# Kernel tuning notes

Hardware: AMD Instinct MI355X
Metric: run time of the kernel (lower is better)

Reference implementation:

```python
import jax, jax.numpy as jnp
import numpy as np

N_NODES = 50000
N_EDGES = 800000
D = 128


def _gcn_conv(x, edge_index, W, b):
    """PyG GCNConv: out = D^{-1/2} (A + I) D^{-1/2} (x W) + b.

    edge_index[0] = source nodes, edge_index[1] = target nodes.
    Self-loops handled analytically instead of materializing them.
    """
    n = x.shape[0]
    src, dst = edge_index[0], edge_index[1]
    h = x @ W  # [N, out]
    # degree with self-loop: in-degree of target + 1
    deg = jax.ops.segment_sum(jnp.ones_like(dst, dtype=h.dtype), dst, num_segments=n) + 1.0
    dinv = jax.lax.rsqrt(deg)  # deg >= 1, safe
    norm = dinv[src] * dinv[dst]  # [E]
    msgs = norm[:, None] * h[src]  # [E, out]  (the big irregular-gather intermediate)
    agg = jax.ops.segment_sum(msgs, dst, num_segments=n)
    # self-loop contribution: norm = dinv[i]*dinv[i] = 1/deg
    agg = agg + h * (1.0 / deg)[:, None]
    return agg + b


def setup_inputs() -> dict:
    key = jax.random.key(0)
    k1, k2, k3, k4 = jax.random.split(key, 4)
    x = jax.random.normal(k1, (N_NODES, D), dtype=jnp.float32)
    edge_index = jax.random.randint(k2, (2, N_EDGES), 0, N_NODES, dtype=jnp.int64)
    scale = 1.0 / np.sqrt(D)
    W1 = jax.random.normal(k3, (D, D), dtype=jnp.float32) * scale
    W2 = jax.random.normal(k4, (D, D), dtype=jnp.float32) * scale
    b1 = jnp.zeros((D,), dtype=jnp.float32)
    b2 = jnp.zeros((D,), dtype=jnp.float32)
    return {"x": x, "edge_index": edge_index, "W1": W1, "b1": b1, "W2": W2, "b2": b2}


def reference(x, edge_index, W1, b1, W2, b2):
    h = _gcn_conv(x, edge_index, W1, b1)
    h = jax.nn.relu(h)  # dropout p=0.0 -> identity
    out = _gcn_conv(h, edge_index, W2, b2)
    return out
```

## Files before the change

### kernel.cpp

```cpp
#include <hip/hip_runtime.h>

#define DF 128
#define NBKT_MAX 256
#define CAP 8192
#define SCHUNK 2048

typedef unsigned int uint;
typedef unsigned short ushort;
typedef __attribute__((ext_vector_type(8))) short short8;
typedef __attribute__((ext_vector_type(4))) float f32x4;

union frag_u { uint4 u4; short8 s8; };

__device__ __forceinline__ uint f2u(float f) { return __float_as_uint(f); }
__device__ __forceinline__ ushort rne_bf16(float v) {
    uint u = __float_as_uint(v);
    u = u + 0x7FFFu + ((u >> 16) & 1u);
    return (ushort)(u >> 16);
}
__device__ __forceinline__ float bflo(uint u) { return __uint_as_float(u << 16); }
__device__ __forceinline__ float bfhi(uint u) { return __uint_as_float(u & 0xFFFF0000u); }

__global__ __launch_bounds__(256) void scatter_wprep(const int* __restrict__ src,
                                                     const int* __restrict__ dst,
                                                     int* __restrict__ ccur,
                                                     uint* __restrict__ ebuf,
                                                     int E, int NB, int SB,
                                                     const float* __restrict__ W1,
                                                     const float* __restrict__ W2,
                                                     uint4* __restrict__ Whi,
                                                     uint4* __restrict__ Wlo) {
    __shared__ int cnt[NBKT_MAX];
    __shared__ int base[NBKT_MAX];
    int t = threadIdx.x;
    if ((int)blockIdx.x < SB) {
        int e0 = blockIdx.x * SCHUNK;
        int eb0 = e0 + t * 8;
        int lim = min(E - eb0, 8);
        int d[8], s[8];
        if (lim == 8) {
            int4 d0 = *(const int4*)(dst + eb0), d1 = *(const int4*)(dst + eb0 + 4);
            int4 s0 = *(const int4*)(src + eb0), s1 = *(const int4*)(src + eb0 + 4);
            d[0] = d0.x; d[1] = d0.y; d[2] = d0.z; d[3] = d0.w;
            d[4] = d1.x; d[5] = d1.y; d[6] = d1.z; d[7] = d1.w;
            s[0] = s0.x; s[1] = s0.y; s[2] = s0.z; s[3] = s0.w;
            s[4] = s1.x; s[5] = s1.y; s[6] = s1.z; s[7] = s1.w;
        } else {
            for (int i = 0; i < 8; ++i) { d[i] = 0; s[i] = 0; }
            for (int i = 0; i < lim; ++i) { d[i] = dst[eb0 + i]; s[i] = src[eb0 + i]; }
        }
        for (int i = t; i < NB; i += 256) cnt[i] = 0;
        __syncthreads();
        for (int i = 0; i < 8; ++i)
            if (i < lim) atomicAdd(&cnt[d[i] >> 8], 1);
        __syncthreads();
        for (int i = t; i < NB; i += 256) base[i] = cnt[i] ? atomicAdd(&ccur[i], cnt[i]) : 0;
        __syncthreads();
        for (int i = 0; i < 8; ++i)
            if (i < lim) {
                int b = d[i] >> 8;
                int pos = atomicAdd(&base[b], 1);
                if (pos < CAP) ebuf[(size_t)b * CAP + pos] = ((uint)(d[i] & 255) << 24) | (uint)s[i];
            }
    } else {
        int tt4 = ((int)blockIdx.x - SB) * 256 + t;
        int wsel = tt4 >> 11;
        int tt = tt4 & 2047;
        const float* W = wsel ? W2 : W1;
        int lane = tt & 63;
        int n  = ((tt >> 6) & 7) * 16 + (lane & 15);
        int k0 = (tt >> 9) * 32 + (lane >> 4) * 8;
        uint hi[4], lo[4];
#pragma unroll
        for (int p = 0; p < 4; ++p) {
            float f0 = W[(size_t)(k0 + 2 * p) * DF + n];
            float f1 = W[(size_t)(k0 + 2 * p + 1) * DF + n];
            uint u0 = f2u(f0), u1 = f2u(f1);
            hi[p] = (u1 & 0xFFFF0000u) | (u0 >> 16);
            float l0 = f0 - __uint_as_float(u0 & 0xFFFF0000u);
            float l1 = f1 - __uint_as_float(u1 & 0xFFFF0000u);
            lo[p] = (f2u(l1) & 0xFFFF0000u) | (f2u(l0) >> 16);
        }
        Whi[wsel * 2048 + tt] = make_uint4(hi[0], hi[1], hi[2], hi[3]);
        Wlo[wsel * 2048 + tt] = make_uint4(lo[0], lo[1], lo[2], lo[3]);
    }
}

__global__ __launch_bounds__(256) void sort_gemm1(const uint* __restrict__ ebuf,
                                                  const int* __restrict__ ccur,
                                                  int* __restrict__ rstart,
                                                  int* __restrict__ rend,
                                                  float* __restrict__ dinv,
                                                  ushort* __restrict__ srcs,
                                                  const float* __restrict__ A,
                                                  const uint4* __restrict__ Bhi,
                                                  const uint4* __restrict__ Blo,
                                                  ushort* __restrict__ Hq,
                                                  int NB, int N) {
    __shared__ int cnt[256];
    __shared__ int sp[256];
    int t = threadIdx.x;
    if ((int)blockIdx.x < NB) {
        int b = blockIdx.x;
        int count = min(ccur[b], CAP);
        const uint* eb = ebuf + (size_t)b * CAP;
        cnt[t] = 0;
        __syncthreads();
        for (int j = t; j < count; j += 256) atomicAdd(&cnt[eb[j] >> 24], 1);
        __syncthreads();
        int v = cnt[t];
        int pv = (v + 7) & ~7;
        sp[t] = pv;
        __syncthreads();
        for (int off = 1; off < 256; off <<= 1) {
            int x = (t >= off) ? sp[t - off] : 0;
            __syncthreads();
            sp[t] += x;
            __syncthreads();
        }
        int ex = sp[t] - pv;
        int node = b * 256 + t;
        if (node < N) {
            rstart[node] = b * CAP + ex;
            rend[node]   = b * CAP + ex + v;
            dinv[node] = rsqrtf((float)v + 1.0f);
        }
        sp[t] = ex;
        __syncthreads();
        for (int j = t; j < count; j += 256) {
            uint e = eb[j];
            int pos = atomicAdd(&sp[e >> 24], 1);
            if (pos < CAP) srcs[(size_t)b * CAP + pos] = (ushort)(e & 0xFFFFFFu);
        }
    } else {
        const int lane = t & 63;
        const int w = t >> 6;
        const int l15 = lane & 15, quad = lane >> 4;
        const int rowbase = ((int)blockIdx.x - NB) * 128 + w * 32;
        const int M = N;

        f32x4 acc[2][8];
#pragma unroll
        for (int rt = 0; rt < 2; ++rt)
#pragma unroll
            for (int ct = 0; ct < 8; ++ct) acc[rt][ct] = (f32x4){0.f, 0.f, 0.f, 0.f};

        for (int q = 0; q < 4; ++q) {
            frag_u ah[2], al[2];
#pragma unroll
            for (int rt = 0; rt < 2; ++rt) {
                int m = rowbase + rt * 16 + l15;
                if (m >= M) m = M - 1;
                const float* ap = A + (size_t)m * DF + q * 32 + quad * 8;
                float4 v0 = *(const float4*)ap;
                float4 v1 = *(const float4*)(ap + 4);
                float f[8] = {v0.x, v0.y, v0.z, v0.w, v1.x, v1.y, v1.z, v1.w};
                uint hi[4], lo[4];
#pragma unroll
                for (int p = 0; p < 4; ++p) {
                    uint u0 = f2u(f[2 * p]), u1 = f2u(f[2 * p + 1]);
                    hi[p] = (u1 & 0xFFFF0000u) | (u0 >> 16);
                    float l0 = f[2 * p]     - __uint_as_float(u0 & 0xFFFF0000u);
                    float l1 = f[2 * p + 1] - __uint_as_float(u1 & 0xFFFF0000u);
                    lo[p] = (f2u(l1) & 0xFFFF0000u) | (f2u(l0) >> 16);
                }
                ah[rt].u4 = make_uint4(hi[0], hi[1], hi[2], hi[3]);
                al[rt].u4 = make_uint4(lo[0], lo[1], lo[2], lo[3]);
            }
#pragma unroll
            for (int ct = 0; ct < 8; ++ct) {
                frag_u bh, bl;
                bh.u4 = Bhi[(q * 8 + ct) * 64 + lane];
                bl.u4 = Blo[(q * 8 + ct) * 64 + lane];
#pragma unroll
                for (int rt = 0; rt < 2; ++rt) {
                    acc[rt][ct] = __builtin_amdgcn_mfma_f32_16x16x32_bf16(al[rt].s8, bh.s8, acc[rt][ct], 0, 0, 0);
                    acc[rt][ct] = __builtin_amdgcn_mfma_f32_16x16x32_bf16(ah[rt].s8, bl.s8, acc[rt][ct], 0, 0, 0);
                    acc[rt][ct] = __builtin_amdgcn_mfma_f32_16x16x32_bf16(ah[rt].s8, bh.s8, acc[rt][ct], 0, 0, 0);
                }
            }
        }
#pragma unroll
        for (int rt = 0; rt < 2; ++rt)
#pragma unroll
            for (int reg = 0; reg < 4; ++reg) {
                int row = rowbase + rt * 16 + quad * 4 + reg;
                if (row < M) {
#pragma unroll
                    for (int ct = 0; ct < 8; ++ct)
                        Hq[((size_t)(ct >> 1) * M + row) * 32 + (ct & 1) * 16 + l15] =
                            rne_bf16(acc[rt][ct][reg]);
                }
            }
    }
}

__global__ __launch_bounds__(256) void gemm_bf16A(const ushort* __restrict__ A,
                                                  const uint4* __restrict__ Bhi,
                                                  const uint4* __restrict__ Blo,
                                                  const float* __restrict__ dinv,
                                                  ushort* __restrict__ Hq, int M) {
    const int lane = threadIdx.x & 63;
    const int w = threadIdx.x >> 6;
    const int l15 = lane & 15, quad = lane >> 4;
    const int rowbase = blockIdx.x * 128 + w * 32;

    f32x4 acc[2][8];
#pragma unroll
    for (int rt = 0; rt < 2; ++rt)
#pragma unroll
        for (int ct = 0; ct < 8; ++ct) acc[rt][ct] = (f32x4){0.f, 0.f, 0.f, 0.f};

    for (int q = 0; q < 4; ++q) {
        frag_u a[2];
#pragma unroll
        for (int rt = 0; rt < 2; ++rt) {
            int m = rowbase + rt * 16 + l15;
            if (m >= M) m = M - 1;
            const ushort* ap = A + ((size_t)q * M + m) * 32 + quad * 8;
            a[rt].u4 = *(const uint4*)ap;
        }
#pragma unroll
        for (int ct = 0; ct < 8; ++ct) {
            frag_u bh, bl;
            bh.u4 = Bhi[(q * 8 + ct) * 64 + lane];
            bl.u4 = Blo[(q * 8 + ct) * 64 + lane];
#pragma unroll
            for (int rt = 0; rt < 2; ++rt) {
                acc[rt][ct] = __builtin_amdgcn_mfma_f32_16x16x32_bf16(a[rt].s8, bl.s8, acc[rt][ct], 0, 0, 0);
                acc[rt][ct] = __builtin_amdgcn_mfma_f32_16x16x32_bf16(a[rt].s8, bh.s8, acc[rt][ct], 0, 0, 0);
            }
        }
    }
#pragma unroll
    for (int rt = 0; rt < 2; ++rt)
#pragma unroll
        for (int reg = 0; reg < 4; ++reg) {
            int row = rowbase + rt * 16 + quad * 4 + reg;
            if (row < M) {
                float di = dinv[row];
#pragma unroll
                for (int ct = 0; ct < 8; ++ct)
                    Hq[((size_t)(ct >> 1) * M + row) * 32 + (ct & 1) * 16 + l15] =
                        rne_bf16(acc[rt][ct][reg] * di);
            }
        }
}

template<bool L1>
__global__ __launch_bounds__(256) void quarter_gather(const uint4* __restrict__ H4,
                                                      const float* __restrict__ dinv,
                                                      const int* __restrict__ rstart,
                                                      const int* __restrict__ rend,
                                                      const ushort* __restrict__ srcs,
                                                      const float* __restrict__ bias,
                                                      void* __restrict__ outv, int N) {
    int t = threadIdx.x;
    int bid = blockIdx.x;
    int sub = bid & 7;
    int q = sub >> 1;
    int n = (bid >> 3) * 128 + (sub & 1) * 64 + (t >> 2);
    if (n >= N) return;
    int l = t & 3;
    const uint4* Hq4 = H4 + (size_t)q * N * 4;

    float4 bb0 = ((const float4*)bias)[q * 8 + l * 2];
    float4 bb1 = ((const float4*)bias)[q * 8 + l * 2 + 1];

    float di = dinv[n];
    uint4 self = Hq4[(size_t)n * 4 + l];
    float sc = L1 ? di : 1.0f;
    float a0 = bflo(self.x) * sc, a1 = bfhi(self.x) * sc, a2 = bflo(self.y) * sc, a3 = bfhi(self.y) * sc;
    float a4 = bflo(self.z) * sc, a5 = bfhi(self.z) * sc, a6 = bflo(self.w) * sc, a7 = bfhi(self.w) * sc;

    int j = rstart[n], end = rend[n];
    for (; j + 8 <= end; j += 8) {
        uint4 sv = *(const uint4*)(srcs + j);
        int si[8];
        si[0] = sv.x & 0xFFFF; si[1] = sv.x >> 16;
        si[2] = sv.y & 0xFFFF; si[3] = sv.y >> 16;
        si[4] = sv.z & 0xFFFF; si[5] = sv.z >> 16;
        si[6] = sv.w & 0xFFFF; si[7] = sv.w >> 16;
        uint4 v[8];
#pragma unroll
        for (int i = 0; i < 8; ++i) v[i] = Hq4[(size_t)si[i] * 4 + l];
        if constexpr (L1) {
            float dd[8];
#pragma unroll
            for (int i = 0; i < 8; ++i) dd[i] = dinv[si[i]];
#pragma unroll
            for (int i = 0; i < 8; ++i) {
                a0 = fmaf(bflo(v[i].x), dd[i], a0); a1 = fmaf(bfhi(v[i].x), dd[i], a1);
                a2 = fmaf(bflo(v[i].y), dd[i], a2); a3 = fmaf(bfhi(v[i].y), dd[i], a3);
                a4 = fmaf(bflo(v[i].z), dd[i], a4); a5 = fmaf(bfhi(v[i].z), dd[i], a5);
                a6 = fmaf(bflo(v[i].w), dd[i], a6); a7 = fmaf(bfhi(v[i].w), dd[i], a7);
            }
        } else {
#pragma unroll
            for (int i = 0; i < 8; ++i) {
                a0 += bflo(v[i].x); a1 += bfhi(v[i].x);
                a2 += bflo(v[i].y); a3 += bfhi(v[i].y);
                a4 += bflo(v[i].z); a5 += bfhi(v[i].z);
                a6 += bflo(v[i].w); a7 += bfhi(v[i].w);
            }
        }
    }
    for (; j < end; ++j) {
        int s = srcs[j];
        uint4 v = Hq4[(size_t)s * 4 + l];
        if constexpr (L1) {
            float d = dinv[s];
            a0 = fmaf(bflo(v.x), d, a0); a1 = fmaf(bfhi(v.x), d, a1);
            a2 = fmaf(bflo(v.y), d, a2); a3 = fmaf(bfhi(v.y), d, a3);
            a4 = fmaf(bflo(v.z), d, a4); a5 = fmaf(bfhi(v.z), d, a5);
            a6 = fmaf(bflo(v.w), d, a6); a7 = fmaf(bfhi(v.w), d, a7);
        } else {
            a0 += bflo(v.x); a1 += bfhi(v.x); a2 += bflo(v.y); a3 += bfhi(v.y);
            a4 += bflo(v.z); a5 += bfhi(v.z); a6 += bflo(v.w); a7 += bfhi(v.w);
        }
    }
    float o0 = fmaf(a0, di, bb0.x), o1 = fmaf(a1, di, bb0.y);
    float o2 = fmaf(a2, di, bb0.z), o3 = fmaf(a3, di, bb0.w);
    float o4 = fmaf(a4, di, bb1.x), o5 = fmaf(a5, di, bb1.y);
    float o6 = fmaf(a6, di, bb1.z), o7 = fmaf(a7, di, bb1.w);
    if (L1) {
        o0 = fmaxf(o0, 0.f); o1 = fmaxf(o1, 0.f); o2 = fmaxf(o2, 0.f); o3 = fmaxf(o3, 0.f);
        o4 = fmaxf(o4, 0.f); o5 = fmaxf(o5, 0.f); o6 = fmaxf(o6, 0.f); o7 = fmaxf(o7, 0.f);
        uint4 pk;
        pk.x = (uint)rne_bf16(o0) | ((uint)rne_bf16(o1) << 16);
        pk.y = (uint)rne_bf16(o2) | ((uint)rne_bf16(o3) << 16);
        pk.z = (uint)rne_bf16(o4) | ((uint)rne_bf16(o5) << 16);
        pk.w = (uint)rne_bf16(o6) | ((uint)rne_bf16(o7) << 16);
        ((uint4*)outv)[((size_t)q * N + n) * 4 + l] = pk;
    } else {
        float4* op = (float4*)((float*)outv + (size_t)n * DF + q * 32 + l * 8);
        op[0] = make_float4(o0, o1, o2, o3);
        op[1] = make_float4(o4, o5, o6, o7);
    }
}

extern "C" void kernel_launch(void* const* d_in, const int* in_sizes, int n_in,
                              void* d_out, int out_size, void* d_ws, size_t ws_size,
                              hipStream_t stream) {
    const float* x  = (const float*)d_in[0];
    const int*   ei = (const int*)d_in[1];
    const float* W1 = (const float*)d_in[2];
    const float* b1 = (const float*)d_in[3];
    const float* W2 = (const float*)d_in[4];
    const float* b2 = (const float*)d_in[5];

    const int N = in_sizes[0] / DF;
    const int E = in_sizes[1] / 2;
    const int* src = ei;
    const int* dstp = ei + E;
    const int NB = (N + 255) >> 8;
    const int SB = (E + SCHUNK - 1) / SCHUNK;

    float* out = (float*)d_out;
    char* ws = (char*)d_ws;
    size_t off = 0;
    auto carve = [&](size_t bytes) { void* p = ws + off; off += (bytes + 255) & ~(size_t)255; return p; };
    ushort* Hq     = (ushort*)carve((size_t)N * DF * sizeof(ushort));
    ushort* Z1     = (ushort*)carve((size_t)N * DF * sizeof(ushort));
    float*  dinv   = (float*)carve((size_t)N * sizeof(float));
    int*    rstart = (int*)carve((size_t)N * sizeof(int));
    int*    rend   = (int*)carve((size_t)N * sizeof(int));
    uint*   ebuf   = (uint*)carve((size_t)NB * CAP * sizeof(uint));
    ushort* srcs   = (ushort*)carve((size_t)NB * CAP * sizeof(ushort));
    int*    ccur   = (int*)carve(NBKT_MAX * sizeof(int));
    uint4*  Whi    = (uint4*)carve(2 * 2048 * sizeof(uint4));
    uint4*  Wlo    = (uint4*)carve(2 * 2048 * sizeof(uint4));

    const int gemm_b = (N + 127) / 128;
    const int gath_b = ((N + 127) / 128) * 8;

    hipMemsetAsync(ccur, 0, NBKT_MAX * sizeof(int), stream);
    scatter_wprep<<<SB + 16, 256, 0, stream>>>(src, dstp, ccur, ebuf, E, NB, SB, W1, W2, Whi, Wlo);

    sort_gemm1<<<NB + gemm_b, 256, 0, stream>>>(ebuf, ccur, rstart, rend, dinv, srcs,
                                                x, Whi, Wlo, Hq, NB, N);

    quarter_gather<true><<<gath_b, 256, 0, stream>>>((const uint4*)Hq, dinv, rstart, rend,
                                                     srcs, b1, Z1, N);

    gemm_bf16A<<<gemm_b, 256, 0, stream>>>(Z1, Whi + 2048, Wlo + 2048, dinv, Hq, N);
    quarter_gather<false><<<gath_b, 256, 0, stream>>>((const uint4*)Hq, dinv, rstart, rend,
                                                      srcs, b2, out, N);
}
```

Baseline: 201.3 us.

## Precompute per-edge source dinv in CSR order and split sort into two passes

The bucket sort is split into two kernels, each co-scheduled with half of the first GEMM's blocks. The second pass also writes a per-edge array holding dinv of each source node alongside srcs. The layer-1 gather then reads these contiguous normalisation factors as float4 vectors instead of doing a random dinv lookup per edge, and it prefetches the next group of source indices. This removes irregular dinv gathers at the cost of an extra kernel launch, an extra per-edge float array to write and read, and a re-read of ebuf.

```diff
diff --git a/kernel.cpp b/kernel.cpp
--- a/kernel.cpp
+++ b/kernel.cpp
@@ -86,17 +86,81 @@
     }
 }
 
-__global__ __launch_bounds__(256) void sort_gemm1(const uint* __restrict__ ebuf,
-                                                  const int* __restrict__ ccur,
-                                                  int* __restrict__ rstart,
-                                                  int* __restrict__ rend,
-                                                  float* __restrict__ dinv,
-                                                  ushort* __restrict__ srcs,
-                                                  const float* __restrict__ A,
-                                                  const uint4* __restrict__ Bhi,
-                                                  const uint4* __restrict__ Blo,
-                                                  ushort* __restrict__ Hq,
-                                                  int NB, int N) {
+__device__ __forceinline__ void gemm1_body(int gb, int t,
+                                           const float* __restrict__ A,
+                                           const uint4* __restrict__ Bhi,
+                                           const uint4* __restrict__ Blo,
+                                           ushort* __restrict__ Hq, int M) {
+    const int lane = t & 63;
+    const int w = t >> 6;
+    const int l15 = lane & 15, quad = lane >> 4;
+    const int rowbase = gb * 128 + w * 32;
+
+    f32x4 acc[2][8];
+#pragma unroll
+    for (int rt = 0; rt < 2; ++rt)
+#pragma unroll
+        for (int ct = 0; ct < 8; ++ct) acc[rt][ct] = (f32x4){0.f, 0.f, 0.f, 0.f};
+
+    for (int q = 0; q < 4; ++q) {
+        frag_u ah[2], al[2];
+#pragma unroll
+        for (int rt = 0; rt < 2; ++rt) {
+            int m = rowbase + rt * 16 + l15;
+            if (m >= M) m = M - 1;
+            const float* ap = A + (size_t)m * DF + q * 32 + quad * 8;
+            float4 v0 = *(const float4*)ap;
+            float4 v1 = *(const float4*)(ap + 4);
+            float f[8] = {v0.x, v0.y, v0.z, v0.w, v1.x, v1.y, v1.z, v1.w};
+            uint hi[4], lo[4];
+#pragma unroll
+            for (int p = 0; p < 4; ++p) {
+                uint u0 = f2u(f[2 * p]), u1 = f2u(f[2 * p + 1]);
+                hi[p] = (u1 & 0xFFFF0000u) | (u0 >> 16);
+                float l0 = f[2 * p]     - __uint_as_float(u0 & 0xFFFF0000u);
+                float l1 = f[2 * p + 1] - __uint_as_float(u1 & 0xFFFF0000u);
+                lo[p] = (f2u(l1) & 0xFFFF0000u) | (f2u(l0) >> 16);
+            }
+            ah[rt].u4 = make_uint4(hi[0], hi[1], hi[2], hi[3]);
+            al[rt].u4 = make_uint4(lo[0], lo[1], lo[2], lo[3]);
+        }
+#pragma unroll
+        for (int ct = 0; ct < 8; ++ct) {
+            frag_u bh, bl;
+            bh.u4 = Bhi[(q * 8 + ct) * 64 + lane];
+            bl.u4 = Blo[(q * 8 + ct) * 64 + lane];
+#pragma unroll
+            for (int rt = 0; rt < 2; ++rt) {
+                acc[rt][ct] = __builtin_amdgcn_mfma_f32_16x16x32_bf16(al[rt].s8, bh.s8, acc[rt][ct], 0, 0, 0);
+                acc[rt][ct] = __builtin_amdgcn_mfma_f32_16x16x32_bf16(ah[rt].s8, bl.s8, acc[rt][ct], 0, 0, 0);
+                acc[rt][ct] = __builtin_amdgcn_mfma_f32_16x16x32_bf16(ah[rt].s8, bh.s8, acc[rt][ct], 0, 0, 0);
+            }
+        }
+    }
+#pragma unroll
+    for (int rt = 0; rt < 2; ++rt)
+#pragma unroll
+        for (int reg = 0; reg < 4; ++reg) {
+            int row = rowbase + rt * 16 + quad * 4 + reg;
+            if (row < M) {
+#pragma unroll
+                for (int ct = 0; ct < 8; ++ct)
+                    Hq[((size_t)(ct >> 1) * M + row) * 32 + (ct & 1) * 16 + l15] =
+                        rne_bf16(acc[rt][ct][reg]);
+            }
+        }
+}
+
+__global__ __launch_bounds__(256) void sortA_gemm1(const uint* __restrict__ ebuf,
+                                                   const int* __restrict__ ccur,
+                                                   int* __restrict__ rstart,
+                                                   int* __restrict__ rend,
+                                                   float* __restrict__ dinv,
+                                                   const float* __restrict__ A,
+                                                   const uint4* __restrict__ Bhi,
+                                                   const uint4* __restrict__ Blo,
+                                                   ushort* __restrict__ Hq,
+                                                   int NB, int N) {
     __shared__ int cnt[256];
     __shared__ int sp[256];
     int t = threadIdx.x;
@@ -125,73 +189,42 @@
             rend[node]   = b * CAP + ex + v;
             dinv[node] = rsqrtf((float)v + 1.0f);
         }
-        sp[t] = ex;
+    } else {
+        gemm1_body((int)blockIdx.x - NB, t, A, Bhi, Blo, Hq, N);
+    }
+}
+
+__global__ __launch_bounds__(256) void sortB_gemm1(const uint* __restrict__ ebuf,
+                                                   const int* __restrict__ ccur,
+                                                   const int* __restrict__ rstart,
+                                                   const float* __restrict__ dinv,
+                                                   ushort* __restrict__ srcs,
+                                                   float* __restrict__ srcd,
+                                                   const float* __restrict__ A,
+                                                   const uint4* __restrict__ Bhi,
+                                                   const uint4* __restrict__ Blo,
+                                                   ushort* __restrict__ Hq,
+                                                   int NB, int N, int G1A) {
+    __shared__ int sp[256];
+    int t = threadIdx.x;
+    if ((int)blockIdx.x < NB) {
+        int b = blockIdx.x;
+        int count = min(ccur[b], CAP);
+        const uint* eb = ebuf + (size_t)b * CAP;
+        int node = b * 256 + t;
+        sp[t] = (node < N) ? (rstart[node] - b * CAP) : CAP;
         __syncthreads();
         for (int j = t; j < count; j += 256) {
             uint e = eb[j];
+            int s = (int)(e & 0xFFFFFFu);
             int pos = atomicAdd(&sp[e >> 24], 1);
-            if (pos < CAP) srcs[(size_t)b * CAP + pos] = (ushort)(e & 0xFFFFFFu);
+            if (pos < CAP) {
+                srcs[(size_t)b * CAP + pos] = (ushort)s;
+                srcd[(size_t)b * CAP + pos] = dinv[s];
+            }
         }
     } else {
-        const int lane = t & 63;
-        const int w = t >> 6;
-        const int l15 = lane & 15, quad = lane >> 4;
-        const int rowbase = ((int)blockIdx.x - NB) * 128 + w * 32;
-        const int M = N;
-
-        f32x4 acc[2][8];
-#pragma unroll
-        for (int rt = 0; rt < 2; ++rt)
-#pragma unroll
-            for (int ct = 0; ct < 8; ++ct) acc[rt][ct] = (f32x4){0.f, 0.f, 0.f, 0.f};
-
-        for (int q = 0; q < 4; ++q) {
-            frag_u ah[2], al[2];
-#pragma unroll
-            for (int rt = 0; rt < 2; ++rt) {
-                int m = rowbase + rt * 16 + l15;
-                if (m >= M) m = M - 1;
-                const float* ap = A + (size_t)m * DF + q * 32 + quad * 8;
-                float4 v0 = *(const float4*)ap;
-                float4 v1 = *(const float4*)(ap + 4);
-                float f[8] = {v0.x, v0.y, v0.z, v0.w, v1.x, v1.y, v1.z, v1.w};
-                uint hi[4], lo[4];
-#pragma unroll
-                for (int p = 0; p < 4; ++p) {
-                    uint u0 = f2u(f[2 * p]), u1 = f2u(f[2 * p + 1]);
-                    hi[p] = (u1 & 0xFFFF0000u) | (u0 >> 16);
-                    float l0 = f[2 * p]     - __uint_as_float(u0 & 0xFFFF0000u);
-                    float l1 = f[2 * p + 1] - __uint_as_float(u1 & 0xFFFF0000u);
-                    lo[p] = (f2u(l1) & 0xFFFF0000u) | (f2u(l0) >> 16);
-                }
-                ah[rt].u4 = make_uint4(hi[0], hi[1], hi[2], hi[3]);
-                al[rt].u4 = make_uint4(lo[0], lo[1], lo[2], lo[3]);
-            }
-#pragma unroll
-            for (int ct = 0; ct < 8; ++ct) {
-                frag_u bh, bl;
-                bh.u4 = Bhi[(q * 8 + ct) * 64 + lane];
-                bl.u4 = Blo[(q * 8 + ct) * 64 + lane];
-#pragma unroll
-                for (int rt = 0; rt < 2; ++rt) {
-                    acc[rt][ct] = __builtin_amdgcn_mfma_f32_16x16x32_bf16(al[rt].s8, bh.s8, acc[rt][ct], 0, 0, 0);
-                    acc[rt][ct] = __builtin_amdgcn_mfma_f32_16x16x32_bf16(ah[rt].s8, bl.s8, acc[rt][ct], 0, 0, 0);
-                    acc[rt][ct] = __builtin_amdgcn_mfma_f32_16x16x32_bf16(ah[rt].s8, bh.s8, acc[rt][ct], 0, 0, 0);
-                }
-            }
-        }
-#pragma unroll
-        for (int rt = 0; rt < 2; ++rt)
-#pragma unroll
-            for (int reg = 0; reg < 4; ++reg) {
-                int row = rowbase + rt * 16 + quad * 4 + reg;
-                if (row < M) {
-#pragma unroll
-                    for (int ct = 0; ct < 8; ++ct)
-                        Hq[((size_t)(ct >> 1) * M + row) * 32 + (ct & 1) * 16 + l15] =
-                            rne_bf16(acc[rt][ct][reg]);
-                }
-            }
+        gemm1_body((int)blockIdx.x - NB + G1A, t, A, Bhi, Blo, Hq, N);
     }
 }
 
@@ -253,6 +286,7 @@
                                                       const int* __restrict__ rstart,
                                                       const int* __restrict__ rend,
                                                       const ushort* __restrict__ srcs,
+                                                      const float* __restrict__ srcd,
                                                       const float* __restrict__ bias,
                                                       void* __restrict__ outv, int N) {
     int t = threadIdx.x;
@@ -274,20 +308,24 @@
     float a4 = bflo(self.z) * sc, a5 = bfhi(self.z) * sc, a6 = bflo(self.w) * sc, a7 = bfhi(self.w) * sc;
 
     int j = rstart[n], end = rend[n];
-    for (; j + 8 <= end; j += 8) {
-        uint4 sv = *(const uint4*)(srcs + j);
+    int nfull = (end - j) >> 3;
+    uint4 sv;
+    if (nfull > 0) sv = *(const uint4*)(srcs + j);
+    for (int g = 0; g < nfull; ++g) {
+        uint4 svc = sv;
+        if (g + 1 < nfull) sv = *(const uint4*)(srcs + j + 8);
         int si[8];
-        si[0] = sv.x & 0xFFFF; si[1] = sv.x >> 16;
-        si[2] = sv.y & 0xFFFF; si[3] = sv.y >> 16;
-        si[4] = sv.z & 0xFFFF; si[5] = sv.z >> 16;
-        si[6] = sv.w & 0xFFFF; si[7] = sv.w >> 16;
+        si[0] = svc.x & 0xFFFF; si[1] = svc.x >> 16;
+        si[2] = svc.y & 0xFFFF; si[3] = svc.y >> 16;
+        si[4] = svc.z & 0xFFFF; si[5] = svc.z >> 16;
+        si[6] = svc.w & 0xFFFF; si[7] = svc.w >> 16;
         uint4 v[8];
 #pragma unroll
         for (int i = 0; i < 8; ++i) v[i] = Hq4[(size_t)si[i] * 4 + l];
         if constexpr (L1) {
-            float dd[8];
-#pragma unroll
-            for (int i = 0; i < 8; ++i) dd[i] = dinv[si[i]];
+            float4 dd0 = *(const float4*)(srcd + j);
+            float4 dd1 = *(const float4*)(srcd + j + 4);
+            float dd[8] = {dd0.x, dd0.y, dd0.z, dd0.w, dd1.x, dd1.y, dd1.z, dd1.w};
 #pragma unroll
             for (int i = 0; i < 8; ++i) {
                 a0 = fmaf(bflo(v[i].x), dd[i], a0); a1 = fmaf(bfhi(v[i].x), dd[i], a1);
@@ -304,12 +342,12 @@
                 a6 += bflo(v[i].w); a7 += bfhi(v[i].w);
             }
         }
+        j += 8;
     }
     for (; j < end; ++j) {
-        int s = srcs[j];
-        uint4 v = Hq4[(size_t)s * 4 + l];
+        uint4 v = Hq4[(size_t)srcs[j] * 4 + l];
         if constexpr (L1) {
-            float d = dinv[s];
+            float d = srcd[j];
             a0 = fmaf(bflo(v.x), d, a0); a1 = fmaf(bfhi(v.x), d, a1);
             a2 = fmaf(bflo(v.y), d, a2); a3 = fmaf(bfhi(v.y), d, a3);
             a4 = fmaf(bflo(v.z), d, a4); a5 = fmaf(bfhi(v.z), d, a5);
@@ -367,23 +405,28 @@
     int*    rend   = (int*)carve((size_t)N * sizeof(int));
     uint*   ebuf   = (uint*)carve((size_t)NB * CAP * sizeof(uint));
     ushort* srcs   = (ushort*)carve((size_t)NB * CAP * sizeof(ushort));
+    float*  srcd   = (float*)carve((size_t)NB * CAP * sizeof(float));
     int*    ccur   = (int*)carve(NBKT_MAX * sizeof(int));
     uint4*  Whi    = (uint4*)carve(2 * 2048 * sizeof(uint4));
     uint4*  Wlo    = (uint4*)carve(2 * 2048 * sizeof(uint4));
 
     const int gemm_b = (N + 127) / 128;
+    const int G1A = (gemm_b + 1) / 2;
     const int gath_b = ((N + 127) / 128) * 8;
 
     hipMemsetAsync(ccur, 0, NBKT_MAX * sizeof(int), stream);
     scatter_wprep<<<SB + 16, 256, 0, stream>>>(src, dstp, ccur, ebuf, E, NB, SB, W1, W2, Whi, Wlo);
 
-    sort_gemm1<<<NB + gemm_b, 256, 0, stream>>>(ebuf, ccur, rstart, rend, dinv, srcs,
-                                                x, Whi, Wlo, Hq, NB, N);
+    sortA_gemm1<<<NB + G1A, 256, 0, stream>>>(ebuf, ccur, rstart, rend, dinv,
+                                              x, Whi, Wlo, Hq, NB, N);
+
+    sortB_gemm1<<<NB + (gemm_b - G1A), 256, 0, stream>>>(ebuf, ccur, rstart, dinv, srcs, srcd,
+                                                         x, Whi, Wlo, Hq, NB, N, G1A);
 
     quarter_gather<true><<<gath_b, 256, 0, stream>>>((const uint4*)Hq, dinv, rstart, rend,
-                                                     srcs, b1, Z1, N);
+                                                     srcs, srcd, b1, Z1, N);
 
     gemm_bf16A<<<gemm_b, 256, 0, stream>>>(Z1, Whi + 2048, Wlo + 2048, dinv, Hq, N);
     quarter_gather<false><<<gath_b, 256, 0, stream>>>((const uint4*)Hq, dinv, rstart, rend,
-                                                      srcs, b2, out, N);
-}
+                                                      srcs, srcd, b2, out, N);
+}
```

Result: slower. 209.9 us (+4.3%).
